# Kernel optimization log

Hardware: AMD Instinct MI355X
Metric: run time of the kernel (lower is better)

## Reference

```python
import jax, jax.numpy as jnp
import numpy as np

B, N, E, L, H, FA = 64, 29, 812, 9, 256, 5  # batch, max atoms, edges, layers, hidden, atom types
SCALE = 15.0


def _scatter_add(vals, idx):
    # vals [B,E,D], idx [B,E] -> [B,N,D]  (replaces one-hot multiply + reduce_sum)
    return jax.vmap(lambda v, i: jnp.zeros((N, v.shape[-1]), v.dtype).at[i].add(v))(vals, idx)


def _align(x, mask):
    n = jnp.sum(mask, axis=1, keepdims=True)
    mean = jnp.sum(x, axis=1, keepdims=True) / n
    return (x - mean) * mask


def setup_inputs() -> dict:
    key = jax.random.key(0)
    ks = iter(jax.random.split(key, 32))
    # fully connected edges i != j, same graph per batch element
    pairs = np.array([(i, j) for i in range(N) for j in range(N) if i != j], dtype=np.int32)
    edge_indices = jnp.tile(jnp.asarray(pairs)[None], (B, 1, 1))
    x_in = jax.random.normal(next(ks), (B, N, 3), jnp.float32)
    h_in = jax.random.normal(next(ks), (B, N, FA), jnp.float32)
    t = jax.random.uniform(next(ks), (B, N, 1), jnp.float32)
    node_mask = jnp.ones((B, N, 1), jnp.float32)
    edge_mask = jnp.ones((B, E, 1), jnp.float32)

    def w(k, shape, fan):
        return jax.random.normal(k, shape, jnp.float32) / np.float32(np.sqrt(fan))

    params = dict(
        win_w=w(next(ks), (FA + 1, H), FA + 1), win_b=jnp.zeros((H,), jnp.float32),
        wout_w=w(next(ks), (H, FA + 1), H), wout_b=jnp.zeros((FA + 1,), jnp.float32),
        e_w1=w(next(ks), (L, 2 * H + 2, H), 2 * H + 2), e_b1=jnp.zeros((L, H), jnp.float32),
        e_w2=w(next(ks), (L, H, H), H), e_b2=jnp.zeros((L, H), jnp.float32),
        att_w=w(next(ks), (L, H, 1), H), att_b=jnp.zeros((L, 1), jnp.float32),
        h_w1=w(next(ks), (L, 2 * H, H), 2 * H), h_b1=jnp.zeros((L, H), jnp.float32),
        h_w2=w(next(ks), (L, H, H), H), h_b2=jnp.zeros((L, H), jnp.float32),
        x_w1=w(next(ks), (L, 2 * H + 2, H), 2 * H + 2), x_b1=jnp.zeros((L, H), jnp.float32),
        x_w2=w(next(ks), (L, H, H), H), x_b2=jnp.zeros((L, H), jnp.float32),
        x_w3=w(next(ks), (L, H, 1), H),
    )
    return {"x_in": x_in, "h_in": h_in, "t": t, "node_mask": node_mask,
            "edge_mask": edge_mask, "edge_indices": edge_indices, **params}


def _forward(x_in, h_in, t, node_mask, edge_mask, edge_indices, p):
    bidx = jnp.arange(x_in.shape[0])[:, None]
    idx_i, idx_j = edge_indices[..., 0], edge_indices[..., 1]
    h = jnp.concatenate([h_in, t], axis=-1) @ p["win_w"] + p["win_b"]
    x = x_in
    # global pairwise distances, masked (the `a` feature)
    xi0, xj0 = x[bidx, idx_i], x[bidx, idx_j]
    a = jnp.sqrt(jnp.sum((xi0 - xj0) ** 2, axis=-1, keepdims=True)) * edge_mask
    for l in range(L):
        x_i, x_j = x[bidx, idx_i], x[bidx, idx_j]
        diff = (x_i - x_j) * edge_mask              # [B,E,3]
        d = jnp.sqrt(jnp.sum(diff ** 2, axis=-1, keepdims=True))
        h_i, h_j = h[bidx, idx_i], h[bidx, idx_j]
        feat = jnp.concatenate([h_i, h_j, d ** 2, a], axis=-1)  # [B,E,514]
        # --- update_x ---
        u = jax.nn.silu(feat @ p["x_w1"][l] + p["x_b1"][l])
        u = jax.nn.silu(u @ p["x_w2"][l] + p["x_b2"][l])
        u = jnp.tanh(u @ p["x_w3"][l]) * SCALE      # [B,E,1]
        u = u * diff / (d + 1.0)                    # [B,E,3]
        x = (x + _scatter_add(u, idx_i)) * node_mask
        # --- update_h ---
        m = jax.nn.silu(feat @ p["e_w1"][l] + p["e_b1"][l])
        m = jax.nn.silu(m @ p["e_w2"][l] + p["e_b2"][l])
        e = jax.nn.sigmoid(m @ p["att_w"][l] + p["att_b"][l])
        agg = _scatter_add(e * m, idx_i)            # [B,N,256]
        hm = jax.nn.silu(jnp.concatenate([h, agg], axis=-1) @ p["h_w1"][l] + p["h_b1"][l])
        hm = hm @ p["h_w2"][l] + p["h_b2"][l]
        h = (h + hm) * node_mask
    x_out = _align((x - x_in) * node_mask, node_mask)
    h_out = (h @ p["wout_w"] + p["wout_b"]) * node_mask
    return jnp.concatenate([x_out, h_out[..., :-1]], axis=-1)


def reference(x_in, h_in, t, node_mask, edge_mask, edge_indices,
              win_w, win_b, wout_w, wout_b,
              e_w1, e_b1, e_w2, e_b2, att_w, att_b,
              h_w1, h_b1, h_w2, h_b2,
              x_w1, x_b1, x_w2, x_b2, x_w3):
    p = dict(win_w=win_w, win_b=win_b, wout_w=wout_w, wout_b=wout_b,
             e_w1=e_w1, e_b1=e_b1, e_w2=e_w2, e_b2=e_b2,
             att_w=att_w, att_b=att_b,
             h_w1=h_w1, h_b1=h_b1, h_w2=h_w2, h_b2=h_b2,
             x_w1=x_w1, x_b1=x_b1, x_w2=x_w2, x_b2=x_b2, x_w3=x_w3)
    return _forward(x_in, h_in, t, node_mask, edge_mask, edge_indices, p)
```

## Files before the change

### kernel.cpp

```cpp
#include <hip/hip_runtime.h>
#include <math.h>

#define B_ 64
#define N_ 29
#define E_ 812
#define L_ 9
#define H_ 256
#define FA_ 5
#define BN_ (B_*N_)
#define BE_ (B_*E_)
#define DEG_ 28
#define SCALE_ 15.0f

typedef __attribute__((ext_vector_type(8))) short bf16x8;
typedef __attribute__((ext_vector_type(4))) float f32x4;

__device__ __forceinline__ float sigmoidf_(float v){ return 1.0f/(1.0f+expf(-v)); }
__device__ __forceinline__ float siluf_(float v){ return v/(1.0f+expf(-v)); }
__device__ __forceinline__ float fsilu_(float v){
    float e = __expf(-v);
    return v * __builtin_amdgcn_rcpf(1.0f + e);
}

__device__ __forceinline__ ushort f2bf(float f){
    uint u = __float_as_uint(f);
    u += 0x7fffu + ((u>>16)&1u);
    return (ushort)(u>>16);
}
__device__ __forceinline__ float bf2f(ushort h){ return __uint_as_float(((uint)h)<<16); }

__global__ void k_init_h(const float* __restrict__ h_in, const float* __restrict__ t,
                         const float* __restrict__ win_w, const float* __restrict__ win_b,
                         float* __restrict__ h)
{
    int node = blockIdx.x; int c = threadIdx.x;
    float in[6];
    #pragma unroll
    for (int k=0;k<FA_;k++) in[k] = h_in[node*FA_+k];
    in[5] = t[node];
    float acc = win_b[c];
    #pragma unroll
    for (int k=0;k<6;k++) acc += in[k]*win_w[k*H_+c];
    h[(size_t)node*H_+c] = acc;
}

__global__ void k_init_xa(const float* __restrict__ x_in, const int* __restrict__ eidx,
                          const float* __restrict__ emask, float* __restrict__ x, float* __restrict__ a)
{
    int gid = blockIdx.x*256 + threadIdx.x;
    if (gid < BN_*3) x[gid] = x_in[gid];
    if (gid < BE_) {
        int b = gid / E_;
        int ii = eidx[2*gid], jj = eidx[2*gid+1];
        const float* xi = x_in + (size_t)(b*N_+ii)*3;
        const float* xj = x_in + (size_t)(b*N_+jj)*3;
        float dx = xi[0]-xj[0], dy = xi[1]-xj[1], dz = xi[2]-xj[2];
        a[gid] = sqrtf(dx*dx+dy*dy+dz*dz) * emask[gid];
    }
}

__global__ void k_wprep(const float* __restrict__ xw2, const float* __restrict__ ew2,
                        ushort* __restrict__ WfU, ushort* __restrict__ WfM)
{
    int gid = blockIdx.x*256 + threadIdx.x;
    if (gid >= L_*2*8192) return;
    int lane = gid & 63;
    int rest = gid >> 6;
    int ct = rest & 15; rest >>= 4;
    int ks = rest & 7;  rest >>= 3;
    int p  = rest & 1;  int l = rest >> 1;
    const float* src = (p ? ew2 : xw2) + (size_t)l*H_*H_;
    ushort* dst = (p ? WfM : WfU) + (size_t)l*131072;
    int g = lane>>4, li = lane&15;
    int col = ct*16 + li;
    int kb  = ks*32 + g*8;
    size_t fo = ((size_t)(ks*16+ct)*64 + lane)*8;
    ushort* dh = dst + fo;
    ushort* dl = dst + 65536 + fo;
    #pragma unroll
    for (int j=0;j<8;j++){
        float v = src[(size_t)(kb+j)*H_ + col];
        ushort h = f2bf(v);
        dh[j] = h;
        dl[j] = f2bf(v - bf2f(h));
    }
}

struct GArg { const float* A; const float* Bw; const float* bias; const float* add; const float* rmask; float* C; };
struct GArgs { GArg g[6]; };

template<int ACT>
__global__ __launch_bounds__(256)
void k_gemm64(GArgs args, int M, int Kdim)
{
    const GArg ga = args.g[blockIdx.z];
    __shared__ float As[16*68];
    __shared__ float Bs[16*68];
    const int tid = threadIdx.x;
    const int row0 = blockIdx.x*64;
    const int col0 = blockIdx.y*64;
    const int ty = tid>>4, tx = tid&15;
    const int am = tid>>2, ak = (tid&3)<<2;
    const int bk = tid>>4, bn = (tid&15)<<2;
    float acc[4][4] = {};
    const float* Ap = ga.A + (size_t)min(row0+am, M-1)*Kdim + ak;
    const float* Bp = ga.Bw + (size_t)bk*H_ + col0 + bn;
    for (int k0=0; k0<Kdim; k0+=16) {
        float4 av = *(const float4*)(Ap + k0);
        float4 bv = *(const float4*)(Bp + (size_t)k0*H_);
        __syncthreads();
        As[(ak+0)*68+am]=av.x; As[(ak+1)*68+am]=av.y; As[(ak+2)*68+am]=av.z; As[(ak+3)*68+am]=av.w;
        *(float4*)&Bs[bk*68+bn] = bv;
        __syncthreads();
        #pragma unroll
        for (int k=0;k<16;k++) {
            float4 a4 = *(const float4*)&As[k*68 + (ty<<2)];
            float4 b4 = *(const float4*)&Bs[k*68 + (tx<<2)];
            float aa[4]={a4.x,a4.y,a4.z,a4.w};
            float bb[4]={b4.x,b4.y,b4.z,b4.w};
            #pragma unroll
            for (int i=0;i<4;i++)
                #pragma unroll
                for (int j=0;j<4;j++)
                    acc[i][j] = fmaf(aa[i], bb[j], acc[i][j]);
        }
    }
    const int r0 = row0 + (ty<<2);
    const int c0 = col0 + (tx<<2);
    float4 bias4 = make_float4(0.f,0.f,0.f,0.f);
    if (ga.bias) bias4 = *(const float4*)(ga.bias + c0);
    #pragma unroll
    for (int i=0;i<4;i++) {
        int r = r0+i;
        if (r >= M) break;
        float v0=acc[i][0]+bias4.x, v1=acc[i][1]+bias4.y, v2=acc[i][2]+bias4.z, v3=acc[i][3]+bias4.w;
        if (ga.add) {
            float4 ad = *(const float4*)(ga.add + (size_t)r*H_ + c0);
            v0+=ad.x; v1+=ad.y; v2+=ad.z; v3+=ad.w;
        }
        if (ACT==1) { v0=siluf_(v0); v1=siluf_(v1); v2=siluf_(v2); v3=siluf_(v3); }
        if (ga.rmask) { float mv = ga.rmask[r]; v0*=mv; v1*=mv; v2*=mv; v3*=mv; }
        *(float4*)(ga.C + (size_t)r*H_ + c0) = make_float4(v0,v1,v2,v3);
    }
}

__device__ __forceinline__ void frag_compute(
    const float* __restrict__ Xi, const float* __restrict__ Xj,
    const float* __restrict__ w5p, const float* __restrict__ w6p, const float* __restrict__ bp,
    int ni, int nj, float d2, float av, bool valid,
    int wv, int lane, int g,
    ushort (*fragH)[4][64][8], ushort (*fragL)[4][64][8])
{
    if (valid){
        const float* xi = Xi + (size_t)ni*H_;
        const float* xj = Xj + (size_t)nj*H_;
        #pragma unroll
        for (int ks=0; ks<8; ++ks){
            int kb = ks*32 + g*8;
            float4 i0 = *(const float4*)(xi + kb),  i1 = *(const float4*)(xi + kb + 4);
            float4 j0 = *(const float4*)(xj + kb),  j1 = *(const float4*)(xj + kb + 4);
            float4 w50= *(const float4*)(w5p + kb), w51= *(const float4*)(w5p + kb + 4);
            float4 w60= *(const float4*)(w6p + kb), w61= *(const float4*)(w6p + kb + 4);
            float4 b0 = *(const float4*)(bp + kb),  b1v= *(const float4*)(bp + kb + 4);
            float v[8];
            v[0]=fsilu_(i0.x+j0.x+d2*w50.x+av*w60.x+b0.x);
            v[1]=fsilu_(i0.y+j0.y+d2*w50.y+av*w60.y+b0.y);
            v[2]=fsilu_(i0.z+j0.z+d2*w50.z+av*w60.z+b0.z);
            v[3]=fsilu_(i0.w+j0.w+d2*w50.w+av*w60.w+b0.w);
            v[4]=fsilu_(i1.x+j1.x+d2*w51.x+av*w61.x+b1v.x);
            v[5]=fsilu_(i1.y+j1.y+d2*w51.y+av*w61.y+b1v.y);
            v[6]=fsilu_(i1.z+j1.z+d2*w51.z+av*w61.z+b1v.z);
            v[7]=fsilu_(i1.w+j1.w+d2*w51.w+av*w61.w+b1v.w);
            ushort hh[8], ll[8];
            #pragma unroll
            for (int q=0;q<8;q++){ hh[q]=f2bf(v[q]); ll[q]=f2bf(v[q]-bf2f(hh[q])); }
            *(ushort4*)&fragH[ks][wv][lane][0] = make_ushort4(hh[0],hh[1],hh[2],hh[3]);
            *(ushort4*)&fragH[ks][wv][lane][4] = make_ushort4(hh[4],hh[5],hh[6],hh[7]);
            *(ushort4*)&fragL[ks][wv][lane][0] = make_ushort4(ll[0],ll[1],ll[2],ll[3]);
            *(ushort4*)&fragL[ks][wv][lane][4] = make_ushort4(ll[4],ll[5],ll[6],ll[7]);
        }
    } else {
        ushort4 z4 = make_ushort4(0,0,0,0);
        #pragma unroll
        for (int ks=0; ks<8; ++ks){
            *(ushort4*)&fragH[ks][wv][lane][0] = z4;
            *(ushort4*)&fragH[ks][wv][lane][4] = z4;
            *(ushort4*)&fragL[ks][wv][lane][0] = z4;
            *(ushort4*)&fragL[ks][wv][lane][4] = z4;
        }
    }
}

__device__ __forceinline__ void mfma_lds(
    const ushort (*fragH)[4][64][8], const ushort (*fragL)[4][64][8],
    const ushort* __restrict__ bp, int lane, f32x4 (&acc)[4][4])
{
    #pragma unroll
    for (int ks=0; ks<8; ++ks){
        bf16x8 ah[4], al[4];
        #pragma unroll
        for (int rt=0; rt<4; ++rt){
            ah[rt] = *(const bf16x8*)&fragH[ks][rt][lane][0];
            al[rt] = *(const bf16x8*)&fragL[ks][rt][lane][0];
        }
        #pragma unroll
        for (int ct=0; ct<4; ++ct){
            bf16x8 bh = *(const bf16x8*)(bp + ks*8192 + ct*512);
            bf16x8 bl = *(const bf16x8*)(bp + 65536 + ks*8192 + ct*512);
            #pragma unroll
            for (int rt=0; rt<4; ++rt){
                acc[rt][ct] = __builtin_amdgcn_mfma_f32_16x16x32_bf16(ah[rt], bh, acc[rt][ct], 0,0,0);
                acc[rt][ct] = __builtin_amdgcn_mfma_f32_16x16x32_bf16(al[rt], bh, acc[rt][ct], 0,0,0);
                acc[rt][ct] = __builtin_amdgcn_mfma_f32_16x16x32_bf16(ah[rt], bl, acc[rt][ct], 0,0,0);
            }
        }
    }
}

__global__ __launch_bounds__(256, 2)
void k_edge_mega(const float* __restrict__ XHi, const float* __restrict__ XHj,
                 const float* __restrict__ EHi, const float* __restrict__ EHj,
                 const float* __restrict__ x_cur, const float* __restrict__ a,
                 const int* __restrict__ eidx, const float* __restrict__ emask,
                 const float* __restrict__ nmask,
                 const float* __restrict__ xw512, const float* __restrict__ xw513, const float* __restrict__ xb1,
                 const float* __restrict__ ew512, const float* __restrict__ ew513, const float* __restrict__ eb1,
                 const ushort* __restrict__ WfU, const ushort* __restrict__ WfM,
                 const float* __restrict__ xb2, const float* __restrict__ xw3,
                 const float* __restrict__ eb2, const float* __restrict__ attw,
                 const float* __restrict__ attb,
                 float* __restrict__ x_new, float* __restrict__ agg)
{
    __shared__ __align__(16) ushort fragH[8][4][64][8];
    __shared__ __align__(16) ushort fragL[8][4][64][8];
    __shared__ float pdLds[2][4][64];
    __shared__ float easLds[64];
    __shared__ float cxyz[2*DEG_][3];

    const int tid  = threadIdx.x;
    const int lane = tid & 63;
    const int wv   = tid >> 6;
    const int g    = lane >> 4;
    const int li   = lane & 15;
    const int pb   = blockIdx.x;
    const int n0   = 2*pb;

    const int frow = wv*16 + li;
    const bool valid = (frow < 2*DEG_);
    int ni=0, nj=0; float d2=0.f, av=0.f;
    if (valid){
        int drow = n0 + (frow >= DEG_ ? 1 : 0);
        int bb = drow / N_;
        size_t ge = (size_t)n0*DEG_ + frow;
        int jj = eidx[2*ge+1];
        ni = drow; nj = bb*N_ + jj;
        float em = emask[ge];
        float dx=(x_cur[ni*3+0]-x_cur[nj*3+0])*em;
        float dy=(x_cur[ni*3+1]-x_cur[nj*3+1])*em;
        float dz=(x_cur[ni*3+2]-x_cur[nj*3+2])*em;
        d2 = dx*dx+dy*dy+dz*dz;
        av = a[ge];
    }

    const ushort* bpU = WfU + ((size_t)(wv*4)*64 + lane)*8;
    const ushort* bpM = WfM + ((size_t)(wv*4)*64 + lane)*8;

    f32x4 acc[4][4];

    frag_compute(XHi, XHj, xw512, xw513, xb1, ni, nj, d2, av, valid, wv, lane, g, fragH, fragL);
    __syncthreads();

    #pragma unroll
    for (int rt=0;rt<4;++rt)
        #pragma unroll
        for (int ct=0;ct<4;++ct)
            acc[rt][ct] = (f32x4){0.f,0.f,0.f,0.f};
    mfma_lds(fragH, fragL, bpU, lane, acc);
    {
        float pdv[4][4];
        #pragma unroll
        for (int rt=0;rt<4;++rt)
            #pragma unroll
            for (int rg=0;rg<4;++rg) pdv[rt][rg]=0.f;
        #pragma unroll
        for (int ct=0; ct<4; ++ct){
            const int col = wv*64 + ct*16 + li;
            const float bi = xb2[col];
            const float wvv = xw3[col];
            #pragma unroll
            for (int rt=0; rt<4; ++rt)
                #pragma unroll
                for (int rg=0; rg<4; ++rg)
                    pdv[rt][rg] += fsilu_(acc[rt][ct][rg] + bi)*wvv;
        }
        #pragma unroll
        for (int rt=0;rt<4;++rt)
            #pragma unroll
            for (int rg=0;rg<4;++rg){
                float s = pdv[rt][rg];
                s += __shfl_xor(s, 1, 16);
                s += __shfl_xor(s, 2, 16);
                s += __shfl_xor(s, 4, 16);
                s += __shfl_xor(s, 8, 16);
                if (li==0) pdLds[0][wv][rt*16 + g*4 + rg] = s;
            }
    }
    __syncthreads();

    frag_compute(EHi, EHj, ew512, ew513, eb1, ni, nj, d2, av, valid, wv, lane, g, fragH, fragL);
    __syncthreads();

    #pragma unroll
    for (int rt=0;rt<4;++rt)
        #pragma unroll
        for (int ct=0;ct<4;++ct)
            acc[rt][ct] = (f32x4){0.f,0.f,0.f,0.f};
    mfma_lds(fragH, fragL, bpM, lane, acc);
    {
        float pdv[4][4];
        #pragma unroll
        for (int rt=0;rt<4;++rt)
            #pragma unroll
            for (int rg=0;rg<4;++rg) pdv[rt][rg]=0.f;
        #pragma unroll
        for (int ct=0; ct<4; ++ct){
            const int col = wv*64 + ct*16 + li;
            const float bi = eb2[col];
            const float wvv = attw[col];
            #pragma unroll
            for (int rt=0; rt<4; ++rt)
                #pragma unroll
                for (int rg=0; rg<4; ++rg){
                    float v = fsilu_(acc[rt][ct][rg] + bi);
                    acc[rt][ct][rg] = v;
                    pdv[rt][rg] += v*wvv;
                }
        }
        #pragma unroll
        for (int rt=0;rt<4;++rt)
            #pragma unroll
            for (int rg=0;rg<4;++rg){
                float s = pdv[rt][rg];
                s += __shfl_xor(s, 1, 16);
                s += __shfl_xor(s, 2, 16);
                s += __shfl_xor(s, 4, 16);
                s += __shfl_xor(s, 8, 16);
                if (li==0) pdLds[1][wv][rt*16 + g*4 + rg] = s;
            }
    }
    __syncthreads();

    if (wv == 0){
        int t = lane;
        float ea = 0.f;
        if (t < 2*DEG_){
            float sU = pdLds[0][0][t]+pdLds[0][1][t]+pdLds[0][2][t]+pdLds[0][3][t];
            float sM = pdLds[1][0][t]+pdLds[1][1][t]+pdLds[1][2][t]+pdLds[1][3][t];
            float tsc = tanhf(sU)*SCALE_;
            ea = sigmoidf_(sM + attb[0]);
            size_t ge = (size_t)n0*DEG_ + t;
            int drow = n0 + (t >= DEG_ ? 1 : 0);
            int bb = drow / N_;
            int jj = eidx[2*ge+1];
            int njs = bb*N_ + jj;
            float em = emask[ge];
            float dx=(x_cur[drow*3+0]-x_cur[njs*3+0])*em;
            float dy=(x_cur[drow*3+1]-x_cur[njs*3+1])*em;
            float dz=(x_cur[drow*3+2]-x_cur[njs*3+2])*em;
            float dd = sqrtf(dx*dx+dy*dy+dz*dz);
            float sc = tsc/(dd+1.0f);
            cxyz[t][0]=sc*dx; cxyz[t][1]=sc*dy; cxyz[t][2]=sc*dz;
        }
        easLds[t] = (t < 2*DEG_) ? ea : 0.f;
        if (t == 0 || t == DEG_){
            int node = n0 + (t ? 1 : 0);
            float sx=0.f, sy=0.f, sz=0.f;
            #pragma unroll 4
            for (int k=0;k<DEG_;k++){ sx+=cxyz[t+k][0]; sy+=cxyz[t+k][1]; sz+=cxyz[t+k][2]; }
            float nm = nmask[node];
            x_new[node*3+0]=(x_cur[node*3+0]+sx)*nm;
            x_new[node*3+1]=(x_cur[node*3+1]+sy)*nm;
            x_new[node*3+2]=(x_cur[node*3+2]+sz)*nm;
        }
    }
    __syncthreads();

    float p0[4] = {0.f,0.f,0.f,0.f};
    float p1[4] = {0.f,0.f,0.f,0.f};
    #pragma unroll
    for (int rt=0; rt<4; ++rt){
        #pragma unroll
        for (int rg=0; rg<4; ++rg){
            int row = rt*16 + g*4 + rg;
            float w = easLds[row];
            bool hi = (row >= DEG_);
            #pragma unroll
            for (int ct=0; ct<4; ++ct){
                float xv = w*acc[rt][ct][rg];
                p0[ct] += hi ? 0.f : xv;
                p1[ct] += hi ? xv : 0.f;
            }
        }
    }
    #pragma unroll
    for (int ct=0; ct<4; ++ct){
        p0[ct] += __shfl_xor(p0[ct], 16);
        p0[ct] += __shfl_xor(p0[ct], 32);
        p1[ct] += __shfl_xor(p1[ct], 16);
        p1[ct] += __shfl_xor(p1[ct], 32);
    }
    if (g == 0){
        #pragma unroll
        for (int ct=0; ct<4; ++ct){
            int col = wv*64 + ct*16 + li;
            agg[(size_t)n0*H_ + col]     = p0[ct];
            agg[(size_t)(n0+1)*H_ + col] = p1[ct];
        }
    }
}

__global__ void k_out_x(const float* __restrict__ x, const float* __restrict__ x_in,
                        const float* __restrict__ nmask, float* __restrict__ out)
{
    int b = blockIdx.x; int l = threadIdx.x;
    int row = b*N_ + l;
    float xd0=0.f,xd1=0.f,xd2=0.f,nm=0.f;
    if (l < N_) {
        nm = nmask[row];
        xd0 = (x[(size_t)row*3+0]-x_in[(size_t)row*3+0])*nm;
        xd1 = (x[(size_t)row*3+1]-x_in[(size_t)row*3+1])*nm;
        xd2 = (x[(size_t)row*3+2]-x_in[(size_t)row*3+2])*nm;
    }
    float s0=xd0,s1=xd1,s2=xd2,sn=nm;
    #pragma unroll
    for (int off=32; off; off>>=1) {
        s0+=__shfl_xor(s0,off,64); s1+=__shfl_xor(s1,off,64);
        s2+=__shfl_xor(s2,off,64); sn+=__shfl_xor(sn,off,64);
    }
    float m0=s0/sn, m1=s1/sn, m2=s2/sn;
    if (l < N_) {
        out[(size_t)row*8+0]=(xd0-m0)*nm;
        out[(size_t)row*8+1]=(xd1-m1)*nm;
        out[(size_t)row*8+2]=(xd2-m2)*nm;
    }
}

__global__ void k_out_h(const float* __restrict__ h, const float* __restrict__ wout_w, const float* __restrict__ wout_b,
                        const float* __restrict__ nmask, float* __restrict__ out)
{
    int row = blockIdx.x; int lane = threadIdx.x;
    int c4 = lane<<2;
    float4 hv = *(const float4*)(h + (size_t)row*H_ + c4);
    float p0=0,p1=0,p2=0,p3=0,p4=0;
    float hvv[4] = {hv.x,hv.y,hv.z,hv.w};
    #pragma unroll
    for (int j=0;j<4;j++) {
        int k = c4+j;
        float hval = hvv[j];
        p0 += hval * wout_w[k*6+0];
        p1 += hval * wout_w[k*6+1];
        p2 += hval * wout_w[k*6+2];
        p3 += hval * wout_w[k*6+3];
        p4 += hval * wout_w[k*6+4];
    }
    #pragma unroll
    for (int off=32; off; off>>=1) {
        p0+=__shfl_xor(p0,off,64); p1+=__shfl_xor(p1,off,64); p2+=__shfl_xor(p2,off,64);
        p3+=__shfl_xor(p3,off,64); p4+=__shfl_xor(p4,off,64);
    }
    if (lane==0) {
        float nm = nmask[row];
        out[(size_t)row*8+3] = (p0+wout_b[0])*nm;
        out[(size_t)row*8+4] = (p1+wout_b[1])*nm;
        out[(size_t)row*8+5] = (p2+wout_b[2])*nm;
        out[(size_t)row*8+6] = (p3+wout_b[3])*nm;
        out[(size_t)row*8+7] = (p4+wout_b[4])*nm;
    }
}

extern "C" void kernel_launch(void* const* d_in, const int* in_sizes, int n_in,
                              void* d_out, int out_size, void* d_ws, size_t ws_size,
                              hipStream_t stream)
{
    const float* x_in  = (const float*)d_in[0];
    const float* h_in  = (const float*)d_in[1];
    const float* t     = (const float*)d_in[2];
    const float* nmask = (const float*)d_in[3];
    const float* emask = (const float*)d_in[4];
    const int*   eidx  = (const int*)d_in[5];
    const float* win_w = (const float*)d_in[6];
    const float* win_b = (const float*)d_in[7];
    const float* wout_w= (const float*)d_in[8];
    const float* wout_b= (const float*)d_in[9];
    const float* e_w1  = (const float*)d_in[10];
    const float* e_b1  = (const float*)d_in[11];
    const float* e_w2  = (const float*)d_in[12];
    const float* e_b2  = (const float*)d_in[13];
    const float* att_w = (const float*)d_in[14];
    const float* att_b = (const float*)d_in[15];
    const float* h_w1  = (const float*)d_in[16];
    const float* h_b1  = (const float*)d_in[17];
    const float* h_w2  = (const float*)d_in[18];
    const float* h_b2  = (const float*)d_in[19];
    const float* x_w1  = (const float*)d_in[20];
    const float* x_b1  = (const float*)d_in[21];
    const float* x_w2  = (const float*)d_in[22];
    const float* x_b2  = (const float*)d_in[23];
    const float* x_w3  = (const float*)d_in[24];
    float* out = (float*)d_out;

    char* ws = (char*)d_ws;
    size_t off = 0;
    auto alloc = [&](size_t bytes)->float* {
        float* p = (float*)(ws + off);
        off = (off + bytes + 255) & ~(size_t)255;
        return p;
    };
    float* h    = alloc((size_t)BN_*H_*4);
    float* xA   = alloc((size_t)BN_*3*4);
    float* xB   = alloc((size_t)BN_*3*4);
    float* a    = alloc((size_t)BE_*4);
    float* NB5  = alloc((size_t)5*BN_*H_*4);
    float* agg  = alloc((size_t)BN_*H_*4);
    float* hm1  = alloc((size_t)BN_*H_*4);
    ushort* WfU = (ushort*)alloc((size_t)L_*131072*sizeof(ushort));
    ushort* WfM = (ushort*)alloc((size_t)L_*131072*sizeof(ushort));

    k_init_h<<<BN_, H_, 0, stream>>>(h_in, t, win_w, win_b, h);
    k_init_xa<<<(BE_+255)/256, 256, 0, stream>>>(x_in, eidx, emask, xA, a);
    k_wprep<<<(L_*2*8192+255)/256, 256, 0, stream>>>(x_w2, e_w2, WfU, WfM);

    float* x_cur = xA;
    float* x_new = xB;

    for (int l=0; l<L_; l++) {
        const float* xw1l = x_w1 + (size_t)l*514*H_;
        const float* ew1l = e_w1 + (size_t)l*514*H_;
        const float* hw1l = h_w1 + (size_t)l*512*H_;

        GArgs na = {};
        const float* Bz[5] = { xw1l, xw1l+(size_t)256*H_, ew1l, ew1l+(size_t)256*H_, hw1l };
        for (int z=0;z<5;z++){
            na.g[z].A=h; na.g[z].Bw=Bz[z]; na.g[z].bias=nullptr; na.g[z].add=nullptr;
            na.g[z].rmask=nullptr; na.g[z].C=NB5 + (size_t)z*BN_*H_;
        }
        k_gemm64<0><<<dim3(BN_/64, H_/64, 5),256,0,stream>>>(na, BN_, H_);

        float* XHi=NB5;
        float* XHj=NB5+(size_t)BN_*H_;
        float* EHi=NB5+(size_t)2*BN_*H_;
        float* EHj=NB5+(size_t)3*BN_*H_;
        float* Htop=NB5+(size_t)4*BN_*H_;

        k_edge_mega<<<BN_/2, 256, 0, stream>>>(XHi, XHj, EHi, EHj, x_cur, a,
            eidx, emask, nmask,
            xw1l+(size_t)512*H_, xw1l+(size_t)513*H_, x_b1+(size_t)l*H_,
            ew1l+(size_t)512*H_, ew1l+(size_t)513*H_, e_b1+(size_t)l*H_,
            WfU + (size_t)l*131072, WfM + (size_t)l*131072,
            x_b2+(size_t)l*H_, x_w3+(size_t)l*H_,
            e_b2+(size_t)l*H_, att_w+(size_t)l*H_, att_b+l,
            x_new, agg);

        GArgs ha = {};
        ha.g[0] = { agg, hw1l+(size_t)256*H_, h_b1+(size_t)l*H_, Htop, nullptr, hm1 };
        k_gemm64<1><<<dim3(BN_/64,H_/64,1),256,0,stream>>>(ha, BN_, H_);

        GArgs h2 = {};
        h2.g[0] = { hm1, h_w2+(size_t)l*H_*H_, h_b2+(size_t)l*H_, h, nmask, h };
        k_gemm64<0><<<dim3(BN_/64,H_/64,1),256,0,stream>>>(h2, BN_, H_);

        float* tmp = x_cur; x_cur = x_new; x_new = tmp;
    }

    k_out_x<<<B_,64,0,stream>>>(x_cur, x_in, nmask, out);
    k_out_h<<<BN_,64,0,stream>>>(h, wout_w, wout_b, nmask, out);
}
```

Baseline: 1.205 ms.

## Process one destination node per block in edge kernel instead of two

Each edge-kernel block now handles one node (28 edges padded to 32 rows) instead of two nodes (56 rows padded to 64). The fragment-building work is redistributed so each wave fills one row tile for half the K range, LDS and accumulator footprints halve, and launch bounds rise to allow 4 blocks per CU. The grid doubles to BN blocks. This raises occupancy and parallelism, but every block now streams the full weight tiles for half as many rows, doubling weight reads from cache per edge, and the padding fraction stays similar.

```diff
diff --git a/kernel.cpp b/kernel.cpp
--- a/kernel.cpp
+++ b/kernel.cpp
@@ -148,14 +148,16 @@
     const float* __restrict__ Xi, const float* __restrict__ Xj,
     const float* __restrict__ w5p, const float* __restrict__ w6p, const float* __restrict__ bp,
     int ni, int nj, float d2, float av, bool valid,
-    int wv, int lane, int g,
-    ushort (*fragH)[4][64][8], ushort (*fragL)[4][64][8])
-{
+    int rt, int ks0, int lane,
+    ushort (*fragH)[2][64][8], ushort (*fragL)[2][64][8])
+{
+    const int g = lane >> 4;
     if (valid){
         const float* xi = Xi + (size_t)ni*H_;
         const float* xj = Xj + (size_t)nj*H_;
         #pragma unroll
-        for (int ks=0; ks<8; ++ks){
+        for (int kq=0; kq<4; ++kq){
+            int ks = ks0 + kq;
             int kb = ks*32 + g*8;
             float4 i0 = *(const float4*)(xi + kb),  i1 = *(const float4*)(xi + kb + 4);
             float4 j0 = *(const float4*)(xj + kb),  j1 = *(const float4*)(xj + kb + 4);
@@ -174,32 +176,33 @@
             ushort hh[8], ll[8];
             #pragma unroll
             for (int q=0;q<8;q++){ hh[q]=f2bf(v[q]); ll[q]=f2bf(v[q]-bf2f(hh[q])); }
-            *(ushort4*)&fragH[ks][wv][lane][0] = make_ushort4(hh[0],hh[1],hh[2],hh[3]);
-            *(ushort4*)&fragH[ks][wv][lane][4] = make_ushort4(hh[4],hh[5],hh[6],hh[7]);
-            *(ushort4*)&fragL[ks][wv][lane][0] = make_ushort4(ll[0],ll[1],ll[2],ll[3]);
-            *(ushort4*)&fragL[ks][wv][lane][4] = make_ushort4(ll[4],ll[5],ll[6],ll[7]);
+            *(ushort4*)&fragH[ks][rt][lane][0] = make_ushort4(hh[0],hh[1],hh[2],hh[3]);
+            *(ushort4*)&fragH[ks][rt][lane][4] = make_ushort4(hh[4],hh[5],hh[6],hh[7]);
+            *(ushort4*)&fragL[ks][rt][lane][0] = make_ushort4(ll[0],ll[1],ll[2],ll[3]);
+            *(ushort4*)&fragL[ks][rt][lane][4] = make_ushort4(ll[4],ll[5],ll[6],ll[7]);
         }
     } else {
         ushort4 z4 = make_ushort4(0,0,0,0);
         #pragma unroll
-        for (int ks=0; ks<8; ++ks){
-            *(ushort4*)&fragH[ks][wv][lane][0] = z4;
-            *(ushort4*)&fragH[ks][wv][lane][4] = z4;
-            *(ushort4*)&fragL[ks][wv][lane][0] = z4;
-            *(ushort4*)&fragL[ks][wv][lane][4] = z4;
+        for (int kq=0; kq<4; ++kq){
+            int ks = ks0 + kq;
+            *(ushort4*)&fragH[ks][rt][lane][0] = z4;
+            *(ushort4*)&fragH[ks][rt][lane][4] = z4;
+            *(ushort4*)&fragL[ks][rt][lane][0] = z4;
+            *(ushort4*)&fragL[ks][rt][lane][4] = z4;
         }
     }
 }
 
 __device__ __forceinline__ void mfma_lds(
-    const ushort (*fragH)[4][64][8], const ushort (*fragL)[4][64][8],
-    const ushort* __restrict__ bp, int lane, f32x4 (&acc)[4][4])
+    const ushort (*fragH)[2][64][8], const ushort (*fragL)[2][64][8],
+    const ushort* __restrict__ bp, int lane, f32x4 (&acc)[2][4])
 {
     #pragma unroll
     for (int ks=0; ks<8; ++ks){
-        bf16x8 ah[4], al[4];
-        #pragma unroll
-        for (int rt=0; rt<4; ++rt){
+        bf16x8 ah[2], al[2];
+        #pragma unroll
+        for (int rt=0; rt<2; ++rt){
             ah[rt] = *(const bf16x8*)&fragH[ks][rt][lane][0];
             al[rt] = *(const bf16x8*)&fragL[ks][rt][lane][0];
         }
@@ -208,7 +211,7 @@
             bf16x8 bh = *(const bf16x8*)(bp + ks*8192 + ct*512);
             bf16x8 bl = *(const bf16x8*)(bp + 65536 + ks*8192 + ct*512);
             #pragma unroll
-            for (int rt=0; rt<4; ++rt){
+            for (int rt=0; rt<2; ++rt){
                 acc[rt][ct] = __builtin_amdgcn_mfma_f32_16x16x32_bf16(ah[rt], bh, acc[rt][ct], 0,0,0);
                 acc[rt][ct] = __builtin_amdgcn_mfma_f32_16x16x32_bf16(al[rt], bh, acc[rt][ct], 0,0,0);
                 acc[rt][ct] = __builtin_amdgcn_mfma_f32_16x16x32_bf16(ah[rt], bl, acc[rt][ct], 0,0,0);
@@ -217,7 +220,7 @@
     }
 }
 
-__global__ __launch_bounds__(256, 2)
+__global__ __launch_bounds__(256, 4)
 void k_edge_mega(const float* __restrict__ XHi, const float* __restrict__ XHj,
                  const float* __restrict__ EHi, const float* __restrict__ EHj,
                  const float* __restrict__ x_cur, const float* __restrict__ a,
@@ -231,33 +234,33 @@
                  const float* __restrict__ attb,
                  float* __restrict__ x_new, float* __restrict__ agg)
 {
-    __shared__ __align__(16) ushort fragH[8][4][64][8];
-    __shared__ __align__(16) ushort fragL[8][4][64][8];
-    __shared__ float pdLds[2][4][64];
-    __shared__ float easLds[64];
-    __shared__ float cxyz[2*DEG_][3];
+    __shared__ __align__(16) ushort fragH[8][2][64][8];
+    __shared__ __align__(16) ushort fragL[8][2][64][8];
+    __shared__ float pdLds[2][4][32];
+    __shared__ float easLds[32];
+    __shared__ float cxyz[DEG_][3];
 
     const int tid  = threadIdx.x;
     const int lane = tid & 63;
     const int wv   = tid >> 6;
     const int g    = lane >> 4;
     const int li   = lane & 15;
-    const int pb   = blockIdx.x;
-    const int n0   = 2*pb;
-
-    const int frow = wv*16 + li;
-    const bool valid = (frow < 2*DEG_);
-    int ni=0, nj=0; float d2=0.f, av=0.f;
+    const int rt   = wv & 1;
+    const int ks0  = (wv >> 1)*4;
+    const int n0   = blockIdx.x;
+
+    const int frow = rt*16 + li;
+    const bool valid = (frow < DEG_);
+    int nj=0; float d2=0.f, av=0.f;
     if (valid){
-        int drow = n0 + (frow >= DEG_ ? 1 : 0);
-        int bb = drow / N_;
+        int bb = n0 / N_;
         size_t ge = (size_t)n0*DEG_ + frow;
         int jj = eidx[2*ge+1];
-        ni = drow; nj = bb*N_ + jj;
+        nj = bb*N_ + jj;
         float em = emask[ge];
-        float dx=(x_cur[ni*3+0]-x_cur[nj*3+0])*em;
-        float dy=(x_cur[ni*3+1]-x_cur[nj*3+1])*em;
-        float dz=(x_cur[ni*3+2]-x_cur[nj*3+2])*em;
+        float dx=(x_cur[n0*3+0]-x_cur[nj*3+0])*em;
+        float dy=(x_cur[n0*3+1]-x_cur[nj*3+1])*em;
+        float dz=(x_cur[n0*3+2]-x_cur[nj*3+2])*em;
         d2 = dx*dx+dy*dy+dz*dz;
         av = a[ge];
     }
@@ -265,156 +268,148 @@
     const ushort* bpU = WfU + ((size_t)(wv*4)*64 + lane)*8;
     const ushort* bpM = WfM + ((size_t)(wv*4)*64 + lane)*8;
 
-    f32x4 acc[4][4];
-
-    frag_compute(XHi, XHj, xw512, xw513, xb1, ni, nj, d2, av, valid, wv, lane, g, fragH, fragL);
+    f32x4 acc[2][4];
+
+    frag_compute(XHi, XHj, xw512, xw513, xb1, n0, nj, d2, av, valid, rt, ks0, lane, fragH, fragL);
     __syncthreads();
 
     #pragma unroll
-    for (int rt=0;rt<4;++rt)
+    for (int r=0;r<2;++r)
         #pragma unroll
         for (int ct=0;ct<4;++ct)
-            acc[rt][ct] = (f32x4){0.f,0.f,0.f,0.f};
+            acc[r][ct] = (f32x4){0.f,0.f,0.f,0.f};
     mfma_lds(fragH, fragL, bpU, lane, acc);
     {
-        float pdv[4][4];
-        #pragma unroll
-        for (int rt=0;rt<4;++rt)
-            #pragma unroll
-            for (int rg=0;rg<4;++rg) pdv[rt][rg]=0.f;
+        float pdv[2][4];
+        #pragma unroll
+        for (int r=0;r<2;++r)
+            #pragma unroll
+            for (int rg=0;rg<4;++rg) pdv[r][rg]=0.f;
         #pragma unroll
         for (int ct=0; ct<4; ++ct){
             const int col = wv*64 + ct*16 + li;
             const float bi = xb2[col];
             const float wvv = xw3[col];
             #pragma unroll
-            for (int rt=0; rt<4; ++rt)
+            for (int r=0; r<2; ++r)
                 #pragma unroll
                 for (int rg=0; rg<4; ++rg)
-                    pdv[rt][rg] += fsilu_(acc[rt][ct][rg] + bi)*wvv;
-        }
-        #pragma unroll
-        for (int rt=0;rt<4;++rt)
+                    pdv[r][rg] += fsilu_(acc[r][ct][rg] + bi)*wvv;
+        }
+        #pragma unroll
+        for (int r=0;r<2;++r)
             #pragma unroll
             for (int rg=0;rg<4;++rg){
-                float s = pdv[rt][rg];
+                float s = pdv[r][rg];
                 s += __shfl_xor(s, 1, 16);
                 s += __shfl_xor(s, 2, 16);
                 s += __shfl_xor(s, 4, 16);
                 s += __shfl_xor(s, 8, 16);
-                if (li==0) pdLds[0][wv][rt*16 + g*4 + rg] = s;
+                if (li==0) pdLds[0][wv][r*16 + g*4 + rg] = s;
             }
     }
     __syncthreads();
 
-    frag_compute(EHi, EHj, ew512, ew513, eb1, ni, nj, d2, av, valid, wv, lane, g, fragH, fragL);
+    frag_compute(EHi, EHj, ew512, ew513, eb1, n0, nj, d2, av, valid, rt, ks0, lane, fragH, fragL);
     __syncthreads();
 
     #pragma unroll
-    for (int rt=0;rt<4;++rt)
+    for (int r=0;r<2;++r)
         #pragma unroll
         for (int ct=0;ct<4;++ct)
-            acc[rt][ct] = (f32x4){0.f,0.f,0.f,0.f};
+            acc[r][ct] = (f32x4){0.f,0.f,0.f,0.f};
     mfma_lds(fragH, fragL, bpM, lane, acc);
     {
-        float pdv[4][4];
-        #pragma unroll
-        for (int rt=0;rt<4;++rt)
-            #pragma unroll
-            for (int rg=0;rg<4;++rg) pdv[rt][rg]=0.f;
+        float pdv[2][4];
+        #pragma unroll
+        for (int r=0;r<2;++r)
+            #pragma unroll
+            for (int rg=0;rg<4;++rg) pdv[r][rg]=0.f;
         #pragma unroll
         for (int ct=0; ct<4; ++ct){
             const int col = wv*64 + ct*16 + li;
             const float bi = eb2[col];
             const float wvv = attw[col];
             #pragma unroll
-            for (int rt=0; rt<4; ++rt)
+            for (int r=0; r<2; ++r)
                 #pragma unroll
                 for (int rg=0; rg<4; ++rg){
-                    float v = fsilu_(acc[rt][ct][rg] + bi);
-                    acc[rt][ct][rg] = v;
-                    pdv[rt][rg] += v*wvv;
+                    float v = fsilu_(acc[r][ct][rg] + bi);
+                    acc[r][ct][rg] = v;
+                    pdv[r][rg] += v*wvv;
                 }
         }
         #pragma unroll
-        for (int rt=0;rt<4;++rt)
+        for (int r=0;r<2;++r)
             #pragma unroll
             for (int rg=0;rg<4;++rg){
-                float s = pdv[rt][rg];
+                float s = pdv[r][rg];
                 s += __shfl_xor(s, 1, 16);
                 s += __shfl_xor(s, 2, 16);
                 s += __shfl_xor(s, 4, 16);
                 s += __shfl_xor(s, 8, 16);
-                if (li==0) pdLds[1][wv][rt*16 + g*4 + rg] = s;
+                if (li==0) pdLds[1][wv][r*16 + g*4 + rg] = s;
             }
     }
     __syncthreads();
 
     if (wv == 0){
         int t = lane;
-        float ea = 0.f;
-        if (t < 2*DEG_){
-            float sU = pdLds[0][0][t]+pdLds[0][1][t]+pdLds[0][2][t]+pdLds[0][3][t];
-            float sM = pdLds[1][0][t]+pdLds[1][1][t]+pdLds[1][2][t]+pdLds[1][3][t];
-            float tsc = tanhf(sU)*SCALE_;
-            ea = sigmoidf_(sM + attb[0]);
-            size_t ge = (size_t)n0*DEG_ + t;
-            int drow = n0 + (t >= DEG_ ? 1 : 0);
-            int bb = drow / N_;
-            int jj = eidx[2*ge+1];
-            int njs = bb*N_ + jj;
-            float em = emask[ge];
-            float dx=(x_cur[drow*3+0]-x_cur[njs*3+0])*em;
-            float dy=(x_cur[drow*3+1]-x_cur[njs*3+1])*em;
-            float dz=(x_cur[drow*3+2]-x_cur[njs*3+2])*em;
-            float dd = sqrtf(dx*dx+dy*dy+dz*dz);
-            float sc = tsc/(dd+1.0f);
-            cxyz[t][0]=sc*dx; cxyz[t][1]=sc*dy; cxyz[t][2]=sc*dz;
-        }
-        easLds[t] = (t < 2*DEG_) ? ea : 0.f;
-        if (t == 0 || t == DEG_){
-            int node = n0 + (t ? 1 : 0);
+        if (t < 32){
+            float ea = 0.f;
+            if (t < DEG_){
+                float sU = pdLds[0][0][t]+pdLds[0][1][t]+pdLds[0][2][t]+pdLds[0][3][t];
+                float sM = pdLds[1][0][t]+pdLds[1][1][t]+pdLds[1][2][t]+pdLds[1][3][t];
+                float tsc = tanhf(sU)*SCALE_;
+                ea = sigmoidf_(sM + attb[0]);
+                size_t ge = (size_t)n0*DEG_ + t;
+                int bb = n0 / N_;
+                int jj = eidx[2*ge+1];
+                int njs = bb*N_ + jj;
+                float em = emask[ge];
+                float dx=(x_cur[n0*3+0]-x_cur[njs*3+0])*em;
+                float dy=(x_cur[n0*3+1]-x_cur[njs*3+1])*em;
+                float dz=(x_cur[n0*3+2]-x_cur[njs*3+2])*em;
+                float dd = sqrtf(dx*dx+dy*dy+dz*dz);
+                float sc = tsc/(dd+1.0f);
+                cxyz[t][0]=sc*dx; cxyz[t][1]=sc*dy; cxyz[t][2]=sc*dz;
+            }
+            easLds[t] = ea;
+        }
+        if (t == 0){
             float sx=0.f, sy=0.f, sz=0.f;
             #pragma unroll 4
-            for (int k=0;k<DEG_;k++){ sx+=cxyz[t+k][0]; sy+=cxyz[t+k][1]; sz+=cxyz[t+k][2]; }
-            float nm = nmask[node];
-            x_new[node*3+0]=(x_cur[node*3+0]+sx)*nm;
-            x_new[node*3+1]=(x_cur[node*3+1]+sy)*nm;
-            x_new[node*3+2]=(x_cur[node*3+2]+sz)*nm;
+            for (int k=0;k<DEG_;k++){ sx+=cxyz[k][0]; sy+=cxyz[k][1]; sz+=cxyz[k][2]; }
+            float nm = nmask[n0];
+            x_new[n0*3+0]=(x_cur[n0*3+0]+sx)*nm;
+            x_new[n0*3+1]=(x_cur[n0*3+1]+sy)*nm;
+            x_new[n0*3+2]=(x_cur[n0*3+2]+sz)*nm;
         }
     }
     __syncthreads();
 
-    float p0[4] = {0.f,0.f,0.f,0.f};
-    float p1[4] = {0.f,0.f,0.f,0.f};
-    #pragma unroll
-    for (int rt=0; rt<4; ++rt){
+    float p[4] = {0.f,0.f,0.f,0.f};
+    #pragma unroll
+    for (int r=0; r<2; ++r){
         #pragma unroll
         for (int rg=0; rg<4; ++rg){
-            int row = rt*16 + g*4 + rg;
+            int row = r*16 + g*4 + rg;
             float w = easLds[row];
-            bool hi = (row >= DEG_);
-            #pragma unroll
-            for (int ct=0; ct<4; ++ct){
-                float xv = w*acc[rt][ct][rg];
-                p0[ct] += hi ? 0.f : xv;
-                p1[ct] += hi ? xv : 0.f;
-            }
+            #pragma unroll
+            for (int ct=0; ct<4; ++ct)
+                p[ct] += w*acc[r][ct][rg];
         }
     }
     #pragma unroll
     for (int ct=0; ct<4; ++ct){
-        p0[ct] += __shfl_xor(p0[ct], 16);
-        p0[ct] += __shfl_xor(p0[ct], 32);
-        p1[ct] += __shfl_xor(p1[ct], 16);
-        p1[ct] += __shfl_xor(p1[ct], 32);
+        p[ct] += __shfl_xor(p[ct], 16);
+        p[ct] += __shfl_xor(p[ct], 32);
     }
     if (g == 0){
         #pragma unroll
         for (int ct=0; ct<4; ++ct){
             int col = wv*64 + ct*16 + li;
-            agg[(size_t)n0*H_ + col]     = p0[ct];
-            agg[(size_t)(n0+1)*H_ + col] = p1[ct];
+            agg[(size_t)n0*H_ + col] = p[ct];
         }
     }
 }
@@ -552,7 +547,7 @@
         float* EHj=NB5+(size_t)3*BN_*H_;
         float* Htop=NB5+(size_t)4*BN_*H_;
 
-        k_edge_mega<<<BN_/2, 256, 0, stream>>>(XHi, XHj, EHi, EHj, x_cur, a,
+        k_edge_mega<<<BN_, 256, 0, stream>>>(XHi, XHj, EHi, EHj, x_cur, a,
             eidx, emask, nmask,
             xw1l+(size_t)512*H_, xw1l+(size_t)513*H_, x_b1+(size_t)l*H_,
             ew1l+(size_t)512*H_, ew1l+(size_t)513*H_, e_b1+(size_t)l*H_,
```

After: 1.166 ms. 1.03x faster.
